# Kernel optimization log

Hardware: AMD Instinct MI355X
Metric: run time of the kernel (lower is better)

Reference implementation:

```python
import jax, jax.numpy as jnp
import numpy as np

B, P, IN_DIM, OUT_DIM = 4, 120000, 4, 64
SPATIAL = (480, 360, 32)
EPS = 1e-5
SLOPE = 0.01  # LeakyReLU default negative slope


def setup_inputs() -> dict:
    key = jax.random.key(0)
    ks = jax.random.split(key, 10)
    pc = jax.random.normal(ks[0], (B, P, IN_DIM), dtype=jnp.float32)
    pc_indices = jax.random.randint(ks[1], (B, P, 3), 0, 32, dtype=jnp.int32)
    W1 = jax.random.normal(ks[2], (IN_DIM, 16), dtype=jnp.float32) * (1.0 / np.sqrt(IN_DIM))
    b1 = jax.random.normal(ks[3], (16,), dtype=jnp.float32) * 0.01
    g1 = jnp.ones((16,), jnp.float32)
    be1 = jnp.zeros((16,), jnp.float32)
    W2 = jax.random.normal(ks[4], (16, OUT_DIM), dtype=jnp.float32) * 0.25
    b2 = jax.random.normal(ks[5], (OUT_DIM,), dtype=jnp.float32) * 0.01
    g2 = jnp.ones((OUT_DIM,), jnp.float32)
    be2 = jnp.zeros((OUT_DIM,), jnp.float32)
    return {"pc": pc, "pc_indices": pc_indices, "W1": W1, "b1": b1, "g1": g1,
            "be1": be1, "W2": W2, "b2": b2, "g2": g2, "be2": be2}


def _bn_lrelu(h, g, b):
    # BatchNorm1d in training mode: batch mean / biased variance over points
    mean = jnp.mean(h, axis=0)
    var = jnp.mean((h - mean) ** 2, axis=0)
    h = (h - mean) / jnp.sqrt(var + EPS) * g + b
    return jnp.where(h >= 0, h, SLOPE * h)


def reference(pc, pc_indices, W1, b1, g1, be1, W2, b2, g2, be2):
    N = B * P
    x = pc.reshape(N, IN_DIM)
    bid = jnp.repeat(jnp.arange(B, dtype=jnp.int32), P)  # batch id padded in front
    coords = jnp.concatenate([bid[:, None], pc_indices.reshape(N, 3)], axis=1)  # [N,4]

    # small MLP (shuffle/recover in the original is a mathematical no-op for outputs)
    h = _bn_lrelu(x @ W1 + b1, g1, be1)
    feat = _bn_lrelu(h @ W2 + b2, g2, be2)  # [N, OUT_DIM]

    # torch.unique(dim=0) == lexicographic sort of linearized voxel keys
    S0, S1, S2 = SPATIAL
    key = (((coords[:, 0] * S0 + coords[:, 1]) * S1 + coords[:, 2]) * S2 + coords[:, 3])
    order = jnp.argsort(key)
    sk = key[order]
    is_first = jnp.concatenate([jnp.ones((1,), bool), sk[1:] != sk[:-1]])
    seg_sorted = (jnp.cumsum(is_first) - 1).astype(jnp.int32)  # segment id per sorted point
    inv = jnp.zeros((N,), jnp.int32).at[order].set(seg_sorted)  # inverse index (unsorted)

    # scatter_max into (padded, fixed-shape) voxel feature table
    voxel_feat = jax.ops.segment_max(feat, inv, num_segments=N)  # [N, OUT_DIM]
    n_uni = seg_sorted[-1] + 1
    valid = jnp.arange(N) < n_uni
    voxel_feat = jnp.where(valid[:, None], voxel_feat, 0.0)
    voxel_ind = jnp.zeros((N, 4), jnp.int32).at[seg_sorted].set(coords[order])

    return voxel_feat, voxel_ind, feat
```

## Files before the change

### kernel.cpp

```cpp
#include <hip/hip_runtime.h>

typedef unsigned int u32;
typedef unsigned long long u64;

#define N_PTS 480000
#define PPB   120000
#define NKEY  131072
#define NBLK_A 256
#define NBLK_B 256
#define NT64   7500
#define SLOPE 0.01f

__device__ __forceinline__ u32 bf16pack(float lo, float hi) {
    u32 a = __float_as_uint(lo), b = __float_as_uint(hi);
    a += 0x7fffu + ((a >> 16) & 1u);
    b += 0x7fffu + ((b >> 16) & 1u);
    return (a >> 16) | (b & 0xffff0000u);
}
__device__ __forceinline__ float bf_lo(u32 v) { return __uint_as_float(v << 16); }
__device__ __forceinline__ float bf_hi(u32 v) { return __uint_as_float(v & 0xffff0000u); }

__global__ __launch_bounds__(256) void kA0(const float* __restrict__ pc,
                                           const int* __restrict__ pidx,
                                           u32* __restrict__ keys,
                                           u32* __restrict__ cnt,
                                           float* __restrict__ pA) {
    int t = threadIdx.x;
    int g = blockIdx.x * 256 + t;
    ((u64*)cnt)[g] = 0ull;

    float a[14];
#pragma unroll
    for (int j = 0; j < 14; ++j) a[j] = 0.f;

    for (int n = g; n < N_PTS; n += NBLK_A * 256) {
        float4 x = ((const float4*)pc)[n];
        a[0] += x.x; a[1] += x.y; a[2] += x.z; a[3] += x.w;
        a[4] += x.x * x.x; a[5] += x.x * x.y; a[6]  += x.x * x.z; a[7]  += x.x * x.w;
        a[8] += x.y * x.y; a[9] += x.y * x.z; a[10] += x.y * x.w;
        a[11] += x.z * x.z; a[12] += x.z * x.w; a[13] += x.w * x.w;

        int i0 = pidx[3 * n], i1 = pidx[3 * n + 1], i2 = pidx[3 * n + 2];
        int bid = n / PPB;
        keys[n] = (u32)(bid * 32768 + i0 * 1024 + i1 * 32 + i2);
    }

    __shared__ float red[256];
    for (int j = 0; j < 14; ++j) {
        red[t] = a[j];
        __syncthreads();
        for (int s = 128; s > 0; s >>= 1) {
            if (t < s) red[t] += red[t + s];
            __syncthreads();
        }
        if (t == 0) pA[j * NBLK_A + blockIdx.x] = red[0];
        __syncthreads();
    }
}

__global__ __launch_bounds__(256, 1) void kB(const float* __restrict__ pc,
                                             const u32* __restrict__ keys,
                                             const float* __restrict__ pA,
                                             const float* __restrict__ W1,
                                             const float* __restrict__ b1,
                                             const float* __restrict__ g1,
                                             const float* __restrict__ be1,
                                             u32* __restrict__ cnt,
                                             float* __restrict__ pB,
                                             float* __restrict__ stats1) {
    int t = threadIdx.x, w = t >> 6, lane = t & 63;
    __shared__ float S[14];
    __shared__ float sW[80];
    __shared__ float sred[4][152];

    for (int q = w; q < 14; q += 4) {
        const float* p = pA + q * NBLK_A;
        float s = p[lane] + p[lane + 64] + p[lane + 128] + p[lane + 192];
        for (int d = 32; d > 0; d >>= 1) s += __shfl_xor(s, d);
        if (lane == 0) S[q] = s;
    }
    __syncthreads();
    if (t < 16) {
        int c = t;
        double w4[4];
#pragma unroll
        for (int i = 0; i < 4; ++i) w4[i] = W1[i * 16 + c];
        double sx[4] = { S[0], S[1], S[2], S[3] };
        auto sxx = [&](int i, int j) -> double {
            if (i > j) { int k = i; i = j; j = k; }
            int base = (i == 0) ? 4 : (i == 1) ? 8 : (i == 2) ? 11 : 13;
            return (double)S[base + (j - i)];
        };
        double su = 0.0;
        for (int i = 0; i < 4; ++i) su += sx[i] * w4[i];
        double q = 0.0;
        for (int i = 0; i < 4; ++i)
            for (int j = 0; j < 4; ++j) q += w4[i] * w4[j] * sxx(i, j);
        double b = (double)b1[c];
        double sum   = su + b * (double)N_PTS;
        double sumsq = q + 2.0 * b * su + (double)N_PTS * b * b;
        double mean = sum / (double)N_PTS;
        double var  = sumsq / (double)N_PTS - mean * mean;
        float inv = rsqrtf((float)(var + 1e-5));
        float sc = g1[c] * inv;
        float sf = be1[c] - (float)mean * sc;
#pragma unroll
        for (int i = 0; i < 4; ++i) sW[c * 4 + i] = W1[i * 16 + c] * sc;
        sW[64 + c] = b1[c] * sc + sf;
        if (blockIdx.x == 0) {
#pragma unroll
            for (int i = 0; i < 4; ++i) stats1[c * 4 + i] = sW[c * 4 + i];
            stats1[64 + c] = sW[64 + c];
        }
    }
    __syncthreads();

    for (int n = blockIdx.x * 256 + t; n < N_PTS; n += NBLK_B * 256)
        atomicAdd(&cnt[keys[n]], 1u);

    float acc[152];
#pragma unroll
    for (int m = 0; m < 152; ++m) acc[m] = 0.f;

    const float4* sW4 = (const float4*)sW;
    for (int n = blockIdx.x * 256 + t; n < N_PTS; n += NBLK_B * 256) {
        float4 x = ((const float4*)pc)[n];
        float h[16];
#pragma unroll
        for (int k = 0; k < 16; ++k) {
            float4 wk = sW4[k];
            float z = x.x * wk.x + x.y * wk.y + x.z * wk.z + x.w * wk.w + sW[64 + k];
            h[k] = (z >= 0.f) ? z : SLOPE * z;
        }
#pragma unroll
        for (int i = 0; i < 16; ++i) acc[i] += h[i];
#pragma unroll
        for (int i = 0; i < 16; ++i)
#pragma unroll
            for (int j = i; j < 16; ++j)
                acc[16 + i * 16 - (i * (i - 1)) / 2 + (j - i)] += h[i] * h[j];
    }

#pragma unroll
    for (int m = 0; m < 152; ++m) {
        float s = acc[m];
        for (int d = 32; d > 0; d >>= 1) s += __shfl_xor(s, d);
        acc[m] = s;
    }
    if (lane == 0) {
#pragma unroll
        for (int m = 0; m < 152; ++m) sred[w][m] = acc[m];
    }
    __syncthreads();
    if (t < 152)
        pB[t * NBLK_B + blockIdx.x] = sred[0][t] + sred[1][t] + sred[2][t] + sred[3][t];
}

__global__ __launch_bounds__(256) void kS1(const u32* __restrict__ cnt,
                                           u32* __restrict__ bsum,
                                           const float* __restrict__ pB,
                                           const float* __restrict__ W2,
                                           const float* __restrict__ b2,
                                           const float* __restrict__ g2,
                                           const float* __restrict__ be2,
                                           float* __restrict__ stats2) {
    int t = threadIdx.x, b = blockIdx.x;
    uint4 c4 = ((const uint4*)cnt)[b * 256 + t];
    u32 cs = c4.x + c4.y + c4.z + c4.w;
    u32 os = (c4.x > 0) + (c4.y > 0) + (c4.z > 0) + (c4.w > 0);
    __shared__ u32 rc[256], ro[256];
    rc[t] = cs; ro[t] = os;
    __syncthreads();
    for (int s = 128; s > 0; s >>= 1) {
        if (t < s) { rc[t] += rc[t + s]; ro[t] += ro[t + s]; }
        __syncthreads();
    }
    if (t == 0) { bsum[2 * b] = rc[0]; bsum[2 * b + 1] = ro[0]; }

    if (b == 0) {
        int w = t >> 6, lane = t & 63;
        __shared__ float S[152];
        for (int q = w; q < 152; q += 4) {
            const float* p = pB + q * NBLK_B;
            float s = p[lane] + p[lane + 64] + p[lane + 128] + p[lane + 192];
            for (int d = 32; d > 0; d >>= 1) s += __shfl_xor(s, d);
            if (lane == 0) S[q] = s;
        }
        __syncthreads();
        if (t < 64) {
            double wv[16];
#pragma unroll
            for (int k = 0; k < 16; ++k) wv[k] = W2[k * 64 + t];
            double sh = 0.0;
            for (int k = 0; k < 16; ++k) sh += wv[k] * (double)S[k];
            auto qidx = [&](int i, int j) { return 16 + i * 16 - (i * (i - 1)) / 2 + (j - i); };
            double q = 0.0;
            for (int i = 0; i < 16; ++i) {
                q += wv[i] * wv[i] * (double)S[qidx(i, i)];
                double t2 = 0.0;
                for (int j = i + 1; j < 16; ++j) t2 += wv[j] * (double)S[qidx(i, j)];
                q += 2.0 * wv[i] * t2;
            }
            double bb = (double)b2[t];
            double sum   = sh + bb * (double)N_PTS;
            double sumsq = q + 2.0 * bb * sh + (double)N_PTS * bb * bb;
            double mean = sum / (double)N_PTS;
            double var  = sumsq / (double)N_PTS - mean * mean;
            float inv = rsqrtf((float)(var + 1e-5));
            float scs = g2[t] * inv;
            float sf = be2[t] - (float)mean * scs;
#pragma unroll
            for (int k = 0; k < 16; ++k) stats2[k * 64 + t] = W2[k * 64 + t] * scs;
            stats2[1024 + t] = b2[t] * scs + sf;
        }
    }
}

__global__ __launch_bounds__(256) void kS2(u32* __restrict__ cnt,
                                           const u32* __restrict__ bsum,
                                           u32* __restrict__ startc,
                                           float* __restrict__ vi,
                                           u32* __restrict__ nuni) {
    int t = threadIdx.x, b = blockIdx.x;
    __shared__ u32 sbc[128], sbo[128];
    __shared__ u32 cOff, oOff;
    __shared__ u64 scan[256];
    if (t < 128) { sbc[t] = bsum[2 * t]; sbo[t] = bsum[2 * t + 1]; }

    uint4 c4 = ((const uint4*)cnt)[b * 256 + t];
    u32 cv[4] = { c4.x, c4.y, c4.z, c4.w };
    u32 cs = cv[0] + cv[1] + cv[2] + cv[3];
    u32 os = (cv[0] > 0) + (cv[1] > 0) + (cv[2] > 0) + (cv[3] > 0);
    scan[t] = ((u64)cs << 32) | (u64)os;
    __syncthreads();
    if (t == 0) {
        u32 a = 0, o = 0;
        for (int i = 0; i < b; ++i) { a += sbc[i]; o += sbo[i]; }
        cOff = a; oOff = o;
    }
    for (int d = 1; d < 256; d <<= 1) {
        u64 v = (t >= d) ? scan[t - d] : 0ull;
        __syncthreads();
        scan[t] += v;
        __syncthreads();
    }
    u64 ex = scan[t] - (((u64)cs << 32) | (u64)os);
    u32 start = cOff + (u32)(ex >> 32);
    u32 rank  = oOff + (u32)(ex & 0xffffffffull);

    int kbase = b * 1024 + t * 4;
#pragma unroll
    for (int j = 0; j < 4; ++j) {
        u32 k = (u32)(kbase + j);
        cnt[k] = start;
        if (cv[j] > 0) {
            startc[rank] = start;
            float4 o;
            o.x = (float)(k >> 15);
            o.y = (float)((k >> 10) & 31);
            o.z = (float)((k >> 5) & 31);
            o.w = (float)(k & 31);
            ((float4*)vi)[rank] = o;
            rank++;
        }
        start += cv[j];
    }
    if (b == 127 && t == 255) {
        nuni[0] = rank;
        startc[rank] = N_PTS;
    }
}

__global__ __launch_bounds__(256) void kC(const float* __restrict__ pc,
                                          const u32* __restrict__ keys,
                                          u32* __restrict__ cursor,
                                          u32* __restrict__ pid,
                                          const float* __restrict__ stats1,
                                          const float* __restrict__ stats2,
                                          float* __restrict__ feat_out) {
    int t = threadIdx.x;

    for (int n = blockIdx.x * 256 + t; n < N_PTS; n += 2048 * 256) {
        u32 k = keys[n];
        u32 pos = atomicAdd(&cursor[k], 1u);
        pid[pos] = (u32)n;
    }

    __shared__ u32 shp[64][8];

    int cpair = t & 7, psub = t >> 3;
    float w1a[4], w1b[4], c1a, c1b;
#pragma unroll
    for (int i = 0; i < 4; ++i) {
        w1a[i] = stats1[(2 * cpair) * 4 + i];
        w1b[i] = stats1[(2 * cpair + 1) * 4 + i];
    }
    c1a = stats1[64 + 2 * cpair];
    c1b = stats1[64 + 2 * cpair + 1];

    int c2 = t & 63, pg = t >> 6;
    float w2c[16];
#pragma unroll
    for (int k = 0; k < 16; ++k) w2c[k] = stats2[k * 64 + c2];
    float c2fr = stats2[1024 + c2];

    for (int tile = blockIdx.x; tile < NT64; tile += 2048) {
        int base = tile * 64;
#pragma unroll
        for (int half = 0; half < 2; ++half) {
            int p = psub + 32 * half;
            float4 x = ((const float4*)pc)[base + p];
            float za = x.x * w1a[0] + x.y * w1a[1] + x.z * w1a[2] + x.w * w1a[3] + c1a;
            float zb = x.x * w1b[0] + x.y * w1b[1] + x.z * w1b[2] + x.w * w1b[3] + c1b;
            za = (za >= 0.f) ? za : SLOPE * za;
            zb = (zb >= 0.f) ? zb : SLOPE * zb;
            shp[p][cpair] = bf16pack(za, zb);
        }
        __syncthreads();
#pragma unroll
        for (int j = 0; j < 16; ++j) {
            int p = pg + 4 * j;
            const uint4* row = (const uint4*)&shp[p][0];
            uint4 v0 = row[0], v1 = row[1];
            float f = c2fr;
            f += bf_lo(v0.x) * w2c[0]  + bf_hi(v0.x) * w2c[1];
            f += bf_lo(v0.y) * w2c[2]  + bf_hi(v0.y) * w2c[3];
            f += bf_lo(v0.z) * w2c[4]  + bf_hi(v0.z) * w2c[5];
            f += bf_lo(v0.w) * w2c[6]  + bf_hi(v0.w) * w2c[7];
            f += bf_lo(v1.x) * w2c[8]  + bf_hi(v1.x) * w2c[9];
            f += bf_lo(v1.y) * w2c[10] + bf_hi(v1.y) * w2c[11];
            f += bf_lo(v1.z) * w2c[12] + bf_hi(v1.z) * w2c[13];
            f += bf_lo(v1.w) * w2c[14] + bf_hi(v1.w) * w2c[15];
            float ff = (f >= 0.f) ? f : SLOPE * f;
            feat_out[(size_t)(base + p) * 64 + c2] = ff;
        }
        __syncthreads();
    }
}

__global__ __launch_bounds__(256) void kV(const float* __restrict__ feat,
                                          const u32* __restrict__ pid,
                                          const u32* __restrict__ startc,
                                          const u32* __restrict__ nuni,
                                          float* __restrict__ vf,
                                          float* __restrict__ vi) {
    u32 nu = *nuni;
    int w = threadIdx.x >> 6, lane = threadIdx.x & 63;
    for (u32 r = blockIdx.x * 4 + (u32)w; r < N_PTS; r += 8192) {
        if (r < nu) {
            u32 s = startc[r], e = startc[r + 1];
            float m = -3.4e38f;
            for (u32 i = s; i < e; ++i) {
                u32 p = pid[i];
                m = fmaxf(m, feat[(size_t)p * 64 + lane]);
            }
            vf[(size_t)r * 64 + lane] = m;
        } else {
            vf[(size_t)r * 64 + lane] = 0.f;
            if (lane < 4) vi[(size_t)r * 4 + lane] = 0.f;
        }
    }
}

extern "C" void kernel_launch(void* const* d_in, const int* in_sizes, int n_in,
                              void* d_out, int out_size, void* d_ws, size_t ws_size,
                              hipStream_t stream) {
    const float* pc   = (const float*)d_in[0];
    const int*   pidx = (const int*)d_in[1];
    const float* W1   = (const float*)d_in[2];
    const float* b1   = (const float*)d_in[3];
    const float* g1   = (const float*)d_in[4];
    const float* be1  = (const float*)d_in[5];
    const float* W2   = (const float*)d_in[6];
    const float* b2   = (const float*)d_in[7];
    const float* g2   = (const float*)d_in[8];
    const float* be2  = (const float*)d_in[9];

    float* vf   = (float*)d_out;
    float* vi   = vf + (size_t)N_PTS * 64;
    float* feat = vi + (size_t)N_PTS * 4;

    u32* ws     = (u32*)d_ws;
    u32* keys   = ws;
    u32* cnt    = ws + 480000;
    u32* startc = ws + 611072;
    u32* bsum   = ws + 742148;
    u32* nuni   = ws + 742404;
    u32* pid    = ws + 742420;
    float* pA     = (float*)(ws + 1222420);
    float* stats1 = (float*)(ws + 1226004);
    float* pB     = (float*)(ws + 1226084);
    float* stats2 = (float*)(ws + 1264996);

    kA0<<<NBLK_A, 256, 0, stream>>>(pc, pidx, keys, cnt, pA);
    kB<<<NBLK_B, 256, 0, stream>>>(pc, keys, pA, W1, b1, g1, be1, cnt, pB, stats1);
    kS1<<<128, 256, 0, stream>>>(cnt, bsum, pB, W2, b2, g2, be2, stats2);
    kS2<<<128, 256, 0, stream>>>(cnt, bsum, startc, vi, nuni);
    kC<<<2048, 256, 0, stream>>>(pc, keys, cnt, pid, stats1, stats2, feat);
    kV<<<2048, 256, 0, stream>>>(feat, pid, startc, nuni, vf, vi);
}
```

Measured before the change: 195.6 us.

## Fuse MLP feature computation into voxel max kernel, split point-id scatter

Moves the per-point two-layer MLP evaluation out of the separate feature kernel and into the voxel reduction kernel. Each wave computes a point's features on the fly from its coordinates, using readlane to broadcast the 16 hidden values, and writes the features while taking the max. This removes the read-back of the 123 MB feature array from global memory. The point-id scatter becomes its own one-thread-per-point kernel. In exchange, pc is read through a random gather, the serial per-voxel loop now does much more compute, and the bf16 hidden rounding is replaced by full fp32.

```diff
diff --git a/kernel.cpp b/kernel.cpp
--- a/kernel.cpp
+++ b/kernel.cpp
@@ -8,17 +8,7 @@
 #define NKEY  131072
 #define NBLK_A 256
 #define NBLK_B 256
-#define NT64   7500
 #define SLOPE 0.01f
-
-__device__ __forceinline__ u32 bf16pack(float lo, float hi) {
-    u32 a = __float_as_uint(lo), b = __float_as_uint(hi);
-    a += 0x7fffu + ((a >> 16) & 1u);
-    b += 0x7fffu + ((b >> 16) & 1u);
-    return (a >> 16) | (b & 0xffff0000u);
-}
-__device__ __forceinline__ float bf_lo(u32 v) { return __uint_as_float(v << 16); }
-__device__ __forceinline__ float bf_hi(u32 v) { return __uint_as_float(v & 0xffff0000u); }
 
 __global__ __launch_bounds__(256) void kA0(const float* __restrict__ pc,
                                            const int* __restrict__ pidx,
@@ -271,88 +261,59 @@
     }
 }
 
-__global__ __launch_bounds__(256) void kC(const float* __restrict__ pc,
-                                          const u32* __restrict__ keys,
+__global__ __launch_bounds__(256) void kP(const u32* __restrict__ keys,
                                           u32* __restrict__ cursor,
-                                          u32* __restrict__ pid,
-                                          const float* __restrict__ stats1,
-                                          const float* __restrict__ stats2,
-                                          float* __restrict__ feat_out) {
-    int t = threadIdx.x;
-
-    for (int n = blockIdx.x * 256 + t; n < N_PTS; n += 2048 * 256) {
+                                          u32* __restrict__ pid) {
+    int n = blockIdx.x * 256 + threadIdx.x;
+    if (n < N_PTS) {
         u32 k = keys[n];
         u32 pos = atomicAdd(&cursor[k], 1u);
         pid[pos] = (u32)n;
     }
-
-    __shared__ u32 shp[64][8];
-
-    int cpair = t & 7, psub = t >> 3;
-    float w1a[4], w1b[4], c1a, c1b;
-#pragma unroll
-    for (int i = 0; i < 4; ++i) {
-        w1a[i] = stats1[(2 * cpair) * 4 + i];
-        w1b[i] = stats1[(2 * cpair + 1) * 4 + i];
-    }
-    c1a = stats1[64 + 2 * cpair];
-    c1b = stats1[64 + 2 * cpair + 1];
-
-    int c2 = t & 63, pg = t >> 6;
-    float w2c[16];
-#pragma unroll
-    for (int k = 0; k < 16; ++k) w2c[k] = stats2[k * 64 + c2];
-    float c2fr = stats2[1024 + c2];
-
-    for (int tile = blockIdx.x; tile < NT64; tile += 2048) {
-        int base = tile * 64;
-#pragma unroll
-        for (int half = 0; half < 2; ++half) {
-            int p = psub + 32 * half;
-            float4 x = ((const float4*)pc)[base + p];
-            float za = x.x * w1a[0] + x.y * w1a[1] + x.z * w1a[2] + x.w * w1a[3] + c1a;
-            float zb = x.x * w1b[0] + x.y * w1b[1] + x.z * w1b[2] + x.w * w1b[3] + c1b;
-            za = (za >= 0.f) ? za : SLOPE * za;
-            zb = (zb >= 0.f) ? zb : SLOPE * zb;
-            shp[p][cpair] = bf16pack(za, zb);
-        }
-        __syncthreads();
-#pragma unroll
-        for (int j = 0; j < 16; ++j) {
-            int p = pg + 4 * j;
-            const uint4* row = (const uint4*)&shp[p][0];
-            uint4 v0 = row[0], v1 = row[1];
-            float f = c2fr;
-            f += bf_lo(v0.x) * w2c[0]  + bf_hi(v0.x) * w2c[1];
-            f += bf_lo(v0.y) * w2c[2]  + bf_hi(v0.y) * w2c[3];
-            f += bf_lo(v0.z) * w2c[4]  + bf_hi(v0.z) * w2c[5];
-            f += bf_lo(v0.w) * w2c[6]  + bf_hi(v0.w) * w2c[7];
-            f += bf_lo(v1.x) * w2c[8]  + bf_hi(v1.x) * w2c[9];
-            f += bf_lo(v1.y) * w2c[10] + bf_hi(v1.y) * w2c[11];
-            f += bf_lo(v1.z) * w2c[12] + bf_hi(v1.z) * w2c[13];
-            f += bf_lo(v1.w) * w2c[14] + bf_hi(v1.w) * w2c[15];
-            float ff = (f >= 0.f) ? f : SLOPE * f;
-            feat_out[(size_t)(base + p) * 64 + c2] = ff;
-        }
-        __syncthreads();
-    }
-}
-
-__global__ __launch_bounds__(256) void kV(const float* __restrict__ feat,
+}
+
+__global__ __launch_bounds__(256) void kW(const float* __restrict__ pc,
                                           const u32* __restrict__ pid,
                                           const u32* __restrict__ startc,
                                           const u32* __restrict__ nuni,
+                                          const float* __restrict__ stats1,
+                                          const float* __restrict__ stats2,
+                                          float* __restrict__ feat,
                                           float* __restrict__ vf,
                                           float* __restrict__ vi) {
     u32 nu = *nuni;
     int w = threadIdx.x >> 6, lane = threadIdx.x & 63;
+
+    int k1 = lane & 15;
+    float w1c[4];
+#pragma unroll
+    for (int i = 0; i < 4; ++i) w1c[i] = stats1[k1 * 4 + i];
+    float c1 = stats1[64 + k1];
+
+    float w2c[16];
+#pragma unroll
+    for (int k = 0; k < 16; ++k) w2c[k] = stats2[k * 64 + lane];
+    float c2f = stats2[1024 + lane];
+
     for (u32 r = blockIdx.x * 4 + (u32)w; r < N_PTS; r += 8192) {
         if (r < nu) {
             u32 s = startc[r], e = startc[r + 1];
             float m = -3.4e38f;
             for (u32 i = s; i < e; ++i) {
                 u32 p = pid[i];
-                m = fmaxf(m, feat[(size_t)p * 64 + lane]);
+                float4 x = ((const float4*)pc)[p];
+                float hk = x.x * w1c[0] + x.y * w1c[1] + x.z * w1c[2] + x.w * w1c[3] + c1;
+                hk = (hk >= 0.f) ? hk : SLOPE * hk;
+                u32 hbits = __float_as_uint(hk);
+                float f = c2f;
+#pragma unroll
+                for (int k = 0; k < 16; ++k) {
+                    float hv = __uint_as_float((u32)__builtin_amdgcn_readlane((int)hbits, k));
+                    f += hv * w2c[k];
+                }
+                f = (f >= 0.f) ? f : SLOPE * f;
+                feat[(size_t)p * 64 + lane] = f;
+                m = fmaxf(m, f);
             }
             vf[(size_t)r * 64 + lane] = m;
         } else {
@@ -396,6 +357,6 @@
     kB<<<NBLK_B, 256, 0, stream>>>(pc, keys, pA, W1, b1, g1, be1, cnt, pB, stats1);
     kS1<<<128, 256, 0, stream>>>(cnt, bsum, pB, W2, b2, g2, be2, stats2);
     kS2<<<128, 256, 0, stream>>>(cnt, bsum, startc, vi, nuni);
-    kC<<<2048, 256, 0, stream>>>(pc, keys, cnt, pid, stats1, stats2, feat);
-    kV<<<2048, 256, 0, stream>>>(feat, pid, startc, nuni, vf, vi);
-}
+    kP<<<1875, 256, 0, stream>>>(keys, cnt, pid);
+    kW<<<2048, 256, 0, stream>>>(pc, pid, startc, nuni, stats1, stats2, feat, vf, vi);
+}
```

Result: faster. 191.3 us (-2.2%).
